# Kernel tuning notes

Measured on AMD Instinct MI355X. Metric: run time of the kernel, lower is better.

The kernel has to match this reference:

```python
import jax, jax.numpy as jnp
import numpy as np

NEG_INF = jnp.float32(-1e30)  # stand-in for -inf; relu(-inf) == relu(-1e30) == 0


def setup_inputs() -> dict:
    key = jax.random.key(0)
    ks = jax.random.split(key, 8)
    B, S, E = 4, 4096, 512
    query = jax.random.normal(ks[0], (B, S, E), dtype=jnp.float32)
    k_in = jax.random.normal(ks[1], (B, S, E), dtype=jnp.float32)
    v_in = jax.random.normal(ks[2], (B, S, E), dtype=jnp.float32)
    mask = jax.random.randint(ks[3], (B, S, S), 0, 2) > 0  # bool [B,S,S]
    scale = 1.0 / np.sqrt(E)
    W1 = jax.random.uniform(ks[4], (E, E), jnp.float32, -scale, scale)
    b1 = jax.random.uniform(ks[5], (E,), jnp.float32, -scale, scale)
    W2 = jax.random.uniform(ks[6], (E, E), jnp.float32, -scale, scale)
    b2 = jax.random.uniform(ks[7], (E,), jnp.float32, -scale, scale)
    return {"query": query, "key": k_in, "value": v_in, "mask": mask,
            "W1": W1, "b1": b1, "W2": W2, "b2": b2}


def reference(query, key, value, mask, W1, b1, W2, b2):
    # key projection: nn.Linear -> x @ W.T + b
    k = jnp.einsum('bse,fe->bsf', key, W1) + b1
    # raw dot-product correlation scores [B, S, S]
    scores = jnp.einsum('bqe,bke->bqk', query, k)
    # module forces mask[:, :, 0] = True, then fills ~mask with -inf
    m = mask.at[:, :, 0].set(True)
    scores = jnp.where(m, scores, NEG_INF)
    # ReLU instead of softmax (no normalization); dropout is identity in eval
    alpha = jax.nn.relu(scores)
    # value projection then AV matmul
    v = jnp.einsum('bse,fe->bsf', value, W2) + b2
    out = jnp.einsum('bqk,bke->bqe', alpha, v)
    return out
```

## Files before the change

### kernel.cpp

```cpp
#include <hip/hip_runtime.h>
#include <cstdint>


typedef __bf16 bf16x8 __attribute__((ext_vector_type(8)));
typedef float f32x4 __attribute__((ext_vector_type(4)));

__device__ __forceinline__ unsigned short f2bf(float f) {
  unsigned int u = __float_as_uint(f);
  u += 0x7fffu + ((u >> 16) & 1u);
  return (unsigned short)(u >> 16);
}

__device__ __forceinline__ void async_load16(const void* g, void* l) {
  __builtin_amdgcn_global_load_lds(
      (const __attribute__((address_space(1))) unsigned int*)(uintptr_t)g,
      (__attribute__((address_space(3))) unsigned int*)(unsigned int)(uintptr_t)l,
      16, 0, 0);
}

__global__ void cvt_f32_bf16(const float* __restrict__ in,
                             unsigned short* __restrict__ out, int n4) {
  int i = blockIdx.x * blockDim.x + threadIdx.x;
  if (i < n4) {
    float4 f = ((const float4*)in)[i];
    ushort4 o;
    o.x = f2bf(f.x); o.y = f2bf(f.y); o.z = f2bf(f.z); o.w = f2bf(f.w);
    ((ushort4*)out)[i] = o;
  }
}

template <int EPI>
__global__ void __launch_bounds__(256)
gemm_bt(const unsigned short* __restrict__ A, const unsigned short* __restrict__ B,
        void* __restrict__ Cout, const float* __restrict__ bias,
        const int* __restrict__ mask,
        int M, int N, int K,
        long long strA, long long strB, long long strC, long long strM) {
  __shared__ unsigned short sA[128 * 32];
  __shared__ unsigned short sB[128 * 32];

  const int tid  = threadIdx.x;
  const int lane = tid & 63;
  const int wave = tid >> 6;
  const int bz   = blockIdx.z;
  const int tn0  = blockIdx.x * 128;
  const int tm0  = blockIdx.y * 128;

  const unsigned short* Ab = A + (size_t)bz * strA;
  const unsigned short* Bb = B + (size_t)bz * strB;

  const int ldrow = lane >> 2;
  const int lcol  = (lane & 3) * 8;

  const int wm = (wave >> 1) * 64;
  const int wn = (wave & 1) * 64;
  const int lr = lane & 15;
  const int lq = lane >> 4;

  f32x4 acc[4][4] = {};

  for (int k0 = 0; k0 < K; k0 += 32) {
#pragma unroll
    for (int l = 0; l < 2; ++l) {
      const int row = wave * 32 + l * 16;
      async_load16(Ab + (size_t)(tm0 + row + ldrow) * K + (k0 + lcol), &sA[row * 32]);
      async_load16(Bb + (size_t)(tn0 + row + ldrow) * K + (k0 + lcol), &sB[row * 32]);
    }
    __syncthreads();

    bf16x8 af[4], bfr[4];
#pragma unroll
    for (int t = 0; t < 4; ++t) {
      af[t]  = *(const bf16x8*)&sA[(wm + t * 16 + lr) * 32 + lq * 8];
      bfr[t] = *(const bf16x8*)&sB[(wn + t * 16 + lr) * 32 + lq * 8];
    }
#pragma unroll
    for (int mt = 0; mt < 4; ++mt)
#pragma unroll
      for (int nt = 0; nt < 4; ++nt)
        acc[mt][nt] = __builtin_amdgcn_mfma_f32_16x16x32_bf16(af[mt], bfr[nt],
                                                              acc[mt][nt], 0, 0, 0);
    __syncthreads();
  }

#pragma unroll
  for (int mt = 0; mt < 4; ++mt) {
#pragma unroll
    for (int nt = 0; nt < 4; ++nt) {
#pragma unroll
      for (int r = 0; r < 4; ++r) {
        const int m = tm0 + wm + mt * 16 + lq * 4 + r;
        const int n = tn0 + wn + nt * 16 + lr;
        float v = acc[mt][nt][r];
        if constexpr (EPI == 0) {
          v += bias[n];
          ((unsigned short*)Cout)[(size_t)bz * strC + (size_t)m * N + n] = f2bf(v);
        } else if constexpr (EPI == 1) {
          v += bias[m];
          ((unsigned short*)Cout)[(size_t)bz * strC + (size_t)m * N + n] = f2bf(v);
        } else if constexpr (EPI == 2) {
          const int ok = (n == 0) ? 1 : mask[(size_t)bz * strM + (size_t)m * N + n];
          v = (ok != 0) ? fmaxf(v, 0.f) : 0.f;
          ((unsigned short*)Cout)[(size_t)bz * strC + (size_t)m * N + n] = f2bf(v);
        } else {
          ((float*)Cout)[(size_t)bz * strC + (size_t)m * N + n] = v;
        }
      }
    }
  }
}

extern "C" void kernel_launch(void* const* d_in, const int* in_sizes, int n_in,
                              void* d_out, int out_size, void* d_ws, size_t ws_size,
                              hipStream_t stream) {
  const float* query = (const float*)d_in[0];
  const float* key   = (const float*)d_in[1];
  const float* value = (const float*)d_in[2];
  const int*   mask  = (const int*)d_in[3];
  const float* W1    = (const float*)d_in[4];
  const float* b1    = (const float*)d_in[5];
  const float* W2    = (const float*)d_in[6];
  const float* b2    = (const float*)d_in[7];
  float* out = (float*)d_out;

  constexpr int B = 4, S = 4096, E = 512;
  constexpr long long BSE = (long long)B * S * E;
  constexpr long long SE  = (long long)S * E;
  constexpr long long SS  = (long long)S * S;
  constexpr long long EE  = (long long)E * E;

  char* ws = (char*)d_ws;
  unsigned short* Qb   = (unsigned short*)ws;  ws += BSE * 2;
  unsigned short* Kb   = (unsigned short*)ws;  ws += BSE * 2;
  unsigned short* Vb   = (unsigned short*)ws;  ws += BSE * 2;
  unsigned short* W1b  = (unsigned short*)ws;  ws += EE * 2;
  unsigned short* W2b  = (unsigned short*)ws;  ws += EE * 2;
  unsigned short* Kp   = (unsigned short*)ws;  ws += BSE * 2;
  unsigned short* Vpt  = (unsigned short*)ws;  ws += BSE * 2;
  unsigned short* alph = (unsigned short*)ws;  ws += SS * B * 2;

  cvt_f32_bf16<<<dim3(BSE / 1024), 256, 0, stream>>>(query, Qb, (int)(BSE / 4));
  cvt_f32_bf16<<<dim3(BSE / 1024), 256, 0, stream>>>(key,   Kb, (int)(BSE / 4));
  cvt_f32_bf16<<<dim3(BSE / 1024), 256, 0, stream>>>(value, Vb, (int)(BSE / 4));
  cvt_f32_bf16<<<dim3(EE / 1024),  256, 0, stream>>>(W1, W1b, (int)(EE / 4));
  cvt_f32_bf16<<<dim3(EE / 1024),  256, 0, stream>>>(W2, W2b, (int)(EE / 4));

  gemm_bt<0><<<dim3(E / 128, (B * S) / 128, 1), 256, 0, stream>>>(
      Kb, W1b, Kp, b1, nullptr, B * S, E, E, 0, 0, 0, 0);

  gemm_bt<1><<<dim3(S / 128, E / 128, B), 256, 0, stream>>>(
      W2b, Vb, Vpt, b2, nullptr, E, S, E, 0, SE, SE, 0);

  gemm_bt<2><<<dim3(S / 128, S / 128, B), 256, 0, stream>>>(
      Qb, Kp, alph, nullptr, mask, S, S, E, SE, SE, SS, SS);

  gemm_bt<3><<<dim3(E / 128, S / 128, B), 256, 0, stream>>>(
      alph, Vpt, out, nullptr, nullptr, S, E, S, SS, SE, SE, 0);
}
```

Measured before the change: 746.7 us.

## Fuse score GEMM, mask-ReLU and AV GEMM; pack mask into bitfield

Replaces the separate scores GEMM (which wrote a bf16 alpha matrix of B*S*S) and the AV GEMM with one fused kernel. Each block handles 32 query rows, computes 128-key score tiles in registers, applies mask and ReLU from a prepacked bitmask, stages the result in LDS, and accumulates alpha·V directly. A pack_mask pre-pass turns the int32 mask into bits, forcing column 0 to true. This removes the large alpha write/read round trip, but the fused kernel uses small 32-row tiles, re-reads Q and K from global memory for every key tile, and loads V straight from global memory without LDS staging, so reuse and MFMA utilisation may drop.

After: 952.9 us. 27.6% more time.

```diff
diff --git a/kernel.cpp b/kernel.cpp
--- a/kernel.cpp
+++ b/kernel.cpp
@@ -29,13 +29,27 @@
   }
 }
 
+__global__ void pack_mask(const int* __restrict__ m, unsigned int* __restrict__ bits) {
+  const int lane = threadIdx.x & 63;
+  const size_t wid = ((size_t)blockIdx.x * blockDim.x + threadIdx.x) >> 6;
+  const size_t base = wid * 256;
+  unsigned long long bl[4];
+#pragma unroll
+  for (int c = 0; c < 4; ++c) {
+    size_t e = base + (size_t)c * 64 + lane;
+    int col = (int)(e & 4095);
+    bl[c] = __ballot((m[e] != 0) || (col == 0));
+  }
+  if (lane < 8)
+    bits[base / 32 + lane] = (unsigned int)(bl[lane >> 1] >> ((lane & 1) * 32));
+}
+
 template <int EPI>
 __global__ void __launch_bounds__(256)
 gemm_bt(const unsigned short* __restrict__ A, const unsigned short* __restrict__ B,
         void* __restrict__ Cout, const float* __restrict__ bias,
-        const int* __restrict__ mask,
         int M, int N, int K,
-        long long strA, long long strB, long long strC, long long strM) {
+        long long strA, long long strB, long long strC) {
   __shared__ unsigned short sA[128 * 32];
   __shared__ unsigned short sB[128 * 32];
 
@@ -51,7 +65,6 @@
 
   const int ldrow = lane >> 2;
   const int lcol  = (lane & 3) * 8;
-
   const int wm = (wave >> 1) * 64;
   const int wn = (wave & 1) * 64;
   const int lr = lane & 15;
@@ -84,30 +97,117 @@
   }
 
 #pragma unroll
-  for (int mt = 0; mt < 4; ++mt) {
-#pragma unroll
-    for (int nt = 0; nt < 4; ++nt) {
+  for (int mt = 0; mt < 4; ++mt)
+#pragma unroll
+    for (int nt = 0; nt < 4; ++nt)
 #pragma unroll
       for (int r = 0; r < 4; ++r) {
         const int m = tm0 + wm + mt * 16 + lq * 4 + r;
         const int n = tn0 + wn + nt * 16 + lr;
         float v = acc[mt][nt][r];
-        if constexpr (EPI == 0) {
-          v += bias[n];
-          ((unsigned short*)Cout)[(size_t)bz * strC + (size_t)m * N + n] = f2bf(v);
-        } else if constexpr (EPI == 1) {
-          v += bias[m];
-          ((unsigned short*)Cout)[(size_t)bz * strC + (size_t)m * N + n] = f2bf(v);
-        } else if constexpr (EPI == 2) {
-          const int ok = (n == 0) ? 1 : mask[(size_t)bz * strM + (size_t)m * N + n];
-          v = (ok != 0) ? fmaxf(v, 0.f) : 0.f;
-          ((unsigned short*)Cout)[(size_t)bz * strC + (size_t)m * N + n] = f2bf(v);
-        } else {
-          ((float*)Cout)[(size_t)bz * strC + (size_t)m * N + n] = v;
+        v += (EPI == 0) ? bias[n] : bias[m];
+        ((unsigned short*)Cout)[(size_t)bz * strC + (size_t)m * N + n] = f2bf(v);
+      }
+}
+
+__global__ void __launch_bounds__(256, 2)
+fused_av(const unsigned short* __restrict__ Qb, const unsigned short* __restrict__ Kp,
+         const unsigned short* __restrict__ Vpt, const unsigned int* __restrict__ mbits,
+         float* __restrict__ out) {
+  constexpr int S = 4096, E = 512;
+  __shared__ unsigned short sQ[4 * 32 * 32];
+  __shared__ unsigned short sK[4 * 128 * 32];
+  __shared__ unsigned short sS[4 * 32 * 32];
+
+  const int tid = threadIdx.x;
+  const int lane = tid & 63, w = tid >> 6;
+  const int lr = lane & 15, lq = lane >> 4;
+  const int b = blockIdx.y, q0 = blockIdx.x * 32;
+
+  const unsigned short* Qrow = Qb + ((size_t)b * S + q0) * E;
+  const unsigned short* Kpb  = Kp + (size_t)b * S * E;
+  const unsigned short* Vptb = Vpt + (size_t)b * E * S;
+  const unsigned int*   mb   = mbits + (size_t)b * S * (S / 32);
+
+  f32x4 oacc[2][8] = {};
+
+#pragma unroll 1
+  for (int kt = 0; kt < S / 128; ++kt) {
+    f32x4 sacc[2][2] = {};
+#pragma unroll 1
+    for (int stage = 0; stage < 4; ++stage) {
+      __syncthreads();
+#pragma unroll
+      for (int i = 0; i < 2; ++i) {
+        int f = (tid + i * 256) * 16;
+        int c = f >> 11, row = (f & 2047) >> 6, colb = f & 63;
+        async_load16(Qrow + (size_t)row * E + (stage * 4 + c) * 32 + colb / 2,
+                     (char*)sQ + f);
+      }
+#pragma unroll
+      for (int i = 0; i < 8; ++i) {
+        int f = (tid + i * 256) * 16;
+        int kk = f >> 13, row = (f & 8191) >> 6, colb = f & 63;
+        async_load16(Kpb + (size_t)(kt * 128 + row) * E + stage * 128 + kk * 32 + colb / 2,
+                     (char*)sK + f);
+      }
+      __syncthreads();
+#pragma unroll
+      for (int kk = 0; kk < 4; ++kk) {
+        bf16x8 aq[2], bk[2];
+#pragma unroll
+        for (int mt = 0; mt < 2; ++mt)
+          aq[mt] = *(const bf16x8*)&sQ[(kk * 32 + mt * 16 + lr) * 32 + lq * 8];
+#pragma unroll
+        for (int nt = 0; nt < 2; ++nt)
+          bk[nt] = *(const bf16x8*)&sK[(kk * 128 + w * 32 + nt * 16 + lr) * 32 + lq * 8];
+#pragma unroll
+        for (int mt = 0; mt < 2; ++mt)
+#pragma unroll
+          for (int nt = 0; nt < 2; ++nt)
+            sacc[mt][nt] = __builtin_amdgcn_mfma_f32_16x16x32_bf16(
+                aq[mt], bk[nt], sacc[mt][nt], 0, 0, 0);
+      }
+    }
+#pragma unroll
+    for (int mt = 0; mt < 2; ++mt)
+#pragma unroll
+      for (int r = 0; r < 4; ++r) {
+        const int q = mt * 16 + lq * 4 + r;
+        const unsigned int word = mb[(size_t)(q0 + q) * (S / 32) + kt * 4 + w];
+#pragma unroll
+        for (int nt = 0; nt < 2; ++nt) {
+          float v = sacc[mt][nt][r];
+          v = ((word >> (nt * 16 + lr)) & 1u) ? fmaxf(v, 0.f) : 0.f;
+          sS[(w * 32 + q) * 32 + nt * 16 + lr] = f2bf(v);
         }
       }
-    }
-  }
+    __syncthreads();
+#pragma unroll
+    for (int kk = 0; kk < 4; ++kk) {
+      bf16x8 aS[2];
+#pragma unroll
+      for (int mt = 0; mt < 2; ++mt)
+        aS[mt] = *(const bf16x8*)&sS[(kk * 32 + mt * 16 + lr) * 32 + lq * 8];
+#pragma unroll
+      for (int nt = 0; nt < 8; ++nt) {
+        const bf16x8 bv = *(const bf16x8*)&Vptb[
+            (size_t)(w * 128 + nt * 16 + lr) * S + kt * 128 + kk * 32 + lq * 8];
+#pragma unroll
+        for (int mt = 0; mt < 2; ++mt)
+          oacc[mt][nt] = __builtin_amdgcn_mfma_f32_16x16x32_bf16(
+              aS[mt], bv, oacc[mt][nt], 0, 0, 0);
+      }
+    }
+  }
+#pragma unroll
+  for (int mt = 0; mt < 2; ++mt)
+#pragma unroll
+    for (int nt = 0; nt < 8; ++nt)
+#pragma unroll
+      for (int r = 0; r < 4; ++r)
+        out[((size_t)b * S + q0 + mt * 16 + lq * 4 + r) * E + w * 128 + nt * 16 + lr] =
+            oacc[mt][nt][r];
 }
 
 extern "C" void kernel_launch(void* const* d_in, const int* in_sizes, int n_in,
@@ -126,7 +226,7 @@
   constexpr int B = 4, S = 4096, E = 512;
   constexpr long long BSE = (long long)B * S * E;
   constexpr long long SE  = (long long)S * E;
-  constexpr long long SS  = (long long)S * S;
+  constexpr long long BSS = (long long)B * S * S;
   constexpr long long EE  = (long long)E * E;
 
   char* ws = (char*)d_ws;
@@ -137,7 +237,7 @@
   unsigned short* W2b  = (unsigned short*)ws;  ws += EE * 2;
   unsigned short* Kp   = (unsigned short*)ws;  ws += BSE * 2;
   unsigned short* Vpt  = (unsigned short*)ws;  ws += BSE * 2;
-  unsigned short* alph = (unsigned short*)ws;  ws += SS * B * 2;
+  unsigned int*   mbit = (unsigned int*)ws;    ws += BSS / 8;
 
   cvt_f32_bf16<<<dim3(BSE / 1024), 256, 0, stream>>>(query, Qb, (int)(BSE / 4));
   cvt_f32_bf16<<<dim3(BSE / 1024), 256, 0, stream>>>(key,   Kb, (int)(BSE / 4));
@@ -145,15 +245,12 @@
   cvt_f32_bf16<<<dim3(EE / 1024),  256, 0, stream>>>(W1, W1b, (int)(EE / 4));
   cvt_f32_bf16<<<dim3(EE / 1024),  256, 0, stream>>>(W2, W2b, (int)(EE / 4));
 
+  pack_mask<<<dim3((int)(BSS / 1024)), 256, 0, stream>>>(mask, mbit);
+
   gemm_bt<0><<<dim3(E / 128, (B * S) / 128, 1), 256, 0, stream>>>(
-      Kb, W1b, Kp, b1, nullptr, B * S, E, E, 0, 0, 0, 0);
-
+      Kb, W1b, Kp, b1, B * S, E, E, 0, 0, 0);
   gemm_bt<1><<<dim3(S / 128, E / 128, B), 256, 0, stream>>>(
-      W2b, Vb, Vpt, b2, nullptr, E, S, E, 0, SE, SE, 0);
-
-  gemm_bt<2><<<dim3(S / 128, S / 128, B), 256, 0, stream>>>(
-      Qb, Kp, alph, nullptr, mask, S, S, E, SE, SE, SS, SS);
-
-  gemm_bt<3><<<dim3(E / 128, S / 128, B), 256, 0, stream>>>(
-      alph, Vpt, out, nullptr, nullptr, S, E, S, SS, SE, SE, 0);
-}
+      W2b, Vb, Vpt, b2, E, S, E, 0, SE, SE);
+
+  fused_av<<<dim3(S / 32, B), 256, 0, stream>>>(Qb, Kp, Vpt, mbit, out);
+}
```
